# Optimization experiments

Measured on AMD Instinct MI355X. Metric: run time of the kernel, lower is better.

Reference implementation:

```python
import jax, jax.numpy as jnp
import numpy as np

D_IN = 128
HID = 129
D_H = HID - 1  # ttcn_dim = 128
N, L = 64, 128
NEG = -100000000.0


def setup_inputs() -> dict:
    key = jax.random.key(0)
    ks = jax.random.split(key, 10)
    x_int = jax.random.normal(ks[0], (N, L, D_IN), dtype=jnp.float32)
    mask_x = (jax.random.uniform(ks[1], (N, L, 1)) < 0.7).astype(jnp.float32)
    s1 = 1.0 / np.sqrt(D_IN)
    s2 = 1.0 / np.sqrt(D_H)
    W1 = jax.random.uniform(ks[2], (D_IN, D_H), minval=-s1, maxval=s1, dtype=jnp.float32)
    b1 = jax.random.uniform(ks[3], (D_H,), minval=-s1, maxval=s1, dtype=jnp.float32)
    W2 = jax.random.uniform(ks[4], (D_H, D_H), minval=-s2, maxval=s2, dtype=jnp.float32)
    b2 = jax.random.uniform(ks[5], (D_H,), minval=-s2, maxval=s2, dtype=jnp.float32)
    W3 = jax.random.uniform(ks[6], (D_H, D_IN * D_H), minval=-s2, maxval=s2, dtype=jnp.float32)
    b3 = jax.random.uniform(ks[7], (D_IN * D_H,), minval=-s2, maxval=s2, dtype=jnp.float32)
    t_bias = jax.random.normal(ks[8], (1, D_H), dtype=jnp.float32)
    return {"x_int": x_int, "mask_x": mask_x, "W1": W1, "b1": b1,
            "W2": W2, "b2": b2, "W3": W3, "b3": b3, "t_bias": t_bias}


def reference(x_int, mask_x, W1, b1, W2, b2, W3, b3, t_bias):
    n, lx, _ = x_int.shape
    # filter-generator MLP: (N, L, d_in) -> (N, L, d_in*d_h)
    h = jax.nn.relu(x_int @ W1 + b1)
    h = jax.nn.relu(h @ W2 + b2)
    filt = h @ W3 + b3
    # mask out unobserved timesteps, softmax over the time axis L
    filt = filt * mask_x + (1.0 - mask_x) * NEG
    p = jax.nn.softmax(filt, axis=-2)  # (N, L, d_in*d_h)
    p = p.reshape(n, lx, D_H, D_IN)    # (N, L, d_h, d_in)
    # broadcast-multiply-sum over L and d_in, fused as einsum
    out = jnp.einsum('nlf,nlhf->nh', x_int, p)
    return jax.nn.relu(out + t_bias)
```

## Files before the change

### kernel.cpp

```cpp
#include <hip/hip_runtime.h>

#define NH 16

using hfrag = __attribute__((ext_vector_type(8))) _Float16;
using f4v   = __attribute__((ext_vector_type(4))) float;

__global__ __launch_bounds__(256) void prep_kernel(
    const float* __restrict__ W3, _Float16* __restrict__ w3t,
    const float* __restrict__ x, float* __restrict__ xT,
    const float* __restrict__ maskx, float* __restrict__ xms,
    float* __restrict__ nmask) {
  __shared__ float t[32][33];
  __shared__ float sm2[2][128];
  const int bid = blockIdx.x;
  const int tx = threadIdx.x & 31, ty = threadIdx.x >> 5;
  if (bid < 2048) {
    const int f0 = (bid & 511) * 32;
    const int k0 = (bid >> 9) * 32;
#pragma unroll
    for (int i = 0; i < 4; ++i)
      t[ty + 8 * i][tx] = W3[(size_t)(k0 + ty + 8 * i) * 16384 + f0 + tx];
    __syncthreads();
#pragma unroll
    for (int i = 0; i < 4; ++i)
      w3t[(size_t)(f0 + ty + 8 * i) * 128 + k0 + tx] =
          (_Float16)(t[tx][ty + 8 * i] * 1.44269504f);
  } else if (bid < 3072) {
    const int b2 = bid - 2048;
    const int d0 = (b2 & 3) * 32, l0 = ((b2 >> 2) & 3) * 32, n = b2 >> 4;
    const size_t base = (size_t)n * 16384;
#pragma unroll
    for (int i = 0; i < 4; ++i)
      t[ty + 8 * i][tx] = x[base + (size_t)(l0 + ty + 8 * i) * 128 + d0 + tx];
    __syncthreads();
#pragma unroll
    for (int i = 0; i < 4; ++i)
      xT[base + (size_t)(d0 + ty + 8 * i) * 128 + l0 + tx] = t[tx][ty + 8 * i];
  } else {
    const int n = bid - 3072;
    const int d = threadIdx.x & 127, seg = threadIdx.x >> 7;
    const float* xn = x + (size_t)n * 16384;
    const float* mn = maskx + n * 128;
    float acc = 0.f;
#pragma unroll 8
    for (int l = seg * 64; l < seg * 64 + 64; ++l)
      acc += (mn[l] == 0.f) ? xn[l * 128 + d] : 0.f;
    sm2[seg][d] = acc;
    __syncthreads();
    if (threadIdx.x < 128) xms[n * 128 + d] = sm2[0][d] + sm2[1][d];
    if (threadIdx.x == 0) {
      float c = 0.f;
      for (int l = 0; l < 128; ++l) c += (mn[l] == 0.f) ? 1.f : 0.f;
      nmask[n] = c;
    }
  }
}

__global__ __launch_bounds__(256) void mlp2_kernel(
    const float* __restrict__ x, const float* __restrict__ W1,
    const float* __restrict__ b1, const float* __restrict__ W2,
    const float* __restrict__ b2, const float* __restrict__ maskx,
    _Float16* __restrict__ h2f) {
  __shared__ float wbuf[128 * 128];
  __shared__ float abuf[32 * 132];
  const int n = blockIdx.x, lq = blockIdx.y;
  const int tid = threadIdx.x;

  {
    const float4* wsrc = (const float4*)W1;
    float4* wdst = (float4*)wbuf;
#pragma unroll
    for (int i = 0; i < 16; ++i) wdst[tid + 256 * i] = wsrc[tid + 256 * i];
    const float4* xsrc = (const float4*)(x + (size_t)n * 16384 + lq * 32 * 128);
#pragma unroll
    for (int i = 0; i < 4; ++i) {
      int idx = tid + 256 * i;
      int row = idx >> 5, c4 = idx & 31;
      *(float4*)&abuf[row * 132 + c4 * 4] = xsrc[idx];
    }
  }
  __syncthreads();

  const int tl = tid >> 4, td = tid & 15;
  const int r0 = tl * 2, j0 = td * 8;
  const float m0 = maskx[n * 128 + lq * 32 + r0 + 0];
  const float m1 = maskx[n * 128 + lq * 32 + r0 + 1];
  float s[2][8];

#pragma unroll
  for (int i = 0; i < 2; ++i)
#pragma unroll
    for (int j = 0; j < 8; ++j) s[i][j] = 0.f;
#pragma unroll 4
  for (int k = 0; k < 128; ++k) {
    float a0 = abuf[(r0 + 0) * 132 + k];
    float a1 = abuf[(r0 + 1) * 132 + k];
    float4 bv0 = *(const float4*)&wbuf[k * 128 + j0];
    float4 bv1 = *(const float4*)&wbuf[k * 128 + j0 + 4];
    float b[8] = {bv0.x, bv0.y, bv0.z, bv0.w, bv1.x, bv1.y, bv1.z, bv1.w};
#pragma unroll
    for (int j = 0; j < 8; ++j) {
      s[0][j] += a0 * b[j];
      s[1][j] += a1 * b[j];
    }
  }
  __syncthreads();

#pragma unroll
  for (int i = 0; i < 2; ++i)
#pragma unroll
    for (int j = 0; j < 8; ++j)
      abuf[(r0 + i) * 132 + j0 + j] = fmaxf(s[i][j] + b1[j0 + j], 0.f);
  {
    const float4* wsrc = (const float4*)W2;
    float4* wdst = (float4*)wbuf;
#pragma unroll
    for (int i = 0; i < 16; ++i) wdst[tid + 256 * i] = wsrc[tid + 256 * i];
  }
  __syncthreads();

#pragma unroll
  for (int i = 0; i < 2; ++i)
#pragma unroll
    for (int j = 0; j < 8; ++j) s[i][j] = 0.f;
#pragma unroll 4
  for (int k = 0; k < 128; ++k) {
    float a0 = abuf[(r0 + 0) * 132 + k];
    float a1 = abuf[(r0 + 1) * 132 + k];
    float4 bv0 = *(const float4*)&wbuf[k * 128 + j0];
    float4 bv1 = *(const float4*)&wbuf[k * 128 + j0 + 4];
    float b[8] = {bv0.x, bv0.y, bv0.z, bv0.w, bv1.x, bv1.y, bv1.z, bv1.w};
#pragma unroll
    for (int j = 0; j < 8; ++j) {
      s[0][j] += a0 * b[j];
      s[1][j] += a1 * b[j];
    }
  }

  const float mm[2] = {m0, m1};
  const size_t obase = (size_t)n * 16384 + (size_t)(lq * 32) * 128;
#pragma unroll
  for (int i = 0; i < 2; ++i)
#pragma unroll
    for (int j = 0; j < 8; ++j)
      h2f[obase + (size_t)(r0 + i) * 128 + j0 + j] =
          (_Float16)(fmaxf(s[i][j] + b2[j0 + j], 0.f) * mm[i]);
}

__global__ __launch_bounds__(512, 2) void fused_mfma_kernel(
    const _Float16* __restrict__ h2f, const _Float16* __restrict__ w3t,
    const float* __restrict__ xT, const float* __restrict__ xms,
    const float* __restrict__ nmask, const float* __restrict__ tbias,
    float* __restrict__ out) {
  __shared__ _Float16 aLDS[128 * 128];
  __shared__ float wLDS[8][NH][16];
  const int n = blockIdx.x, hg = blockIdx.y;
  const int tid = threadIdx.x;
  const int wid = tid >> 6, lane = tid & 63;
  const int r = lane & 15, kg = lane >> 4;

  const _Float16* h2n = h2f + (size_t)n * 16384;
  {
    char* lb = (char*)aLDS;
#pragma unroll
    for (int i = 0; i < 4; ++i) {
      const int og = (tid + 512 * i) * 16;
      const int row = og >> 8;
      const int sl = (og >> 4) & 15;
      const float4 v = *(const float4*)((const char*)h2n + og);
      *(float4*)(lb + row * 256 + (sl ^ (row & 7)) * 16) = v;
    }
  }

  f4v xv[8];
  {
    const float* xc =
        xT + (size_t)n * 16384 + (size_t)(wid * 16 + r) * 128 + kg * 4;
#pragma unroll
    for (int rt = 0; rt < 8; ++rt) xv[rt] = *(const f4v*)(xc + rt * 16);
  }
  const float xm = xms[n * 128 + wid * 16 + r];
  const float nm = nmask[n];

  __syncthreads();

  hfrag af[4][8];
  {
    const char* lb = (const char*)aLDS;
#pragma unroll
    for (int ks = 0; ks < 4; ++ks) {
      const int dslByte = ((ks * 4 + kg) ^ (r & 7)) * 16;
#pragma unroll
      for (int rt = 0; rt < 8; ++rt)
        af[ks][rt] = *(const hfrag*)(lb + (rt * 16 + r) * 256 + dslByte);
    }
  }

  const _Float16* w3g =
      w3t + ((size_t)(hg * NH) * 128 + wid * 16 + r) * 128 + kg * 8;
  hfrag bcur[4];
#pragma unroll
  for (int ks = 0; ks < 4; ++ks) bcur[ks] = *(const hfrag*)(w3g + ks * 32);

#pragma unroll 2
  for (int h = 0; h < NH; ++h) {
    f4v acc[8];
#pragma unroll
    for (int rt = 0; rt < 8; ++rt) {
      f4v z = {0.f, 0.f, 0.f, 0.f};
      acc[rt] = __builtin_amdgcn_mfma_f32_16x16x32_f16(af[0][rt], bcur[0], z,
                                                       0, 0, 0);
    }
#pragma unroll
    for (int ks = 1; ks < 4; ++ks)
#pragma unroll
      for (int rt = 0; rt < 8; ++rt)
        acc[rt] = __builtin_amdgcn_mfma_f32_16x16x32_f16(af[ks][rt], bcur[ks],
                                                         acc[rt], 0, 0, 0);

    if (h + 1 < NH) {
      const _Float16* w3n = w3g + (size_t)(h + 1) * 16384;
#pragma unroll
      for (int ks = 0; ks < 4; ++ks) bcur[ks] = *(const hfrag*)(w3n + ks * 32);
    }

    float den0 = 0.f, den1 = 0.f, num0 = 0.f, num1 = 0.f;
#pragma unroll
    for (int rt = 0; rt < 8; rt += 2) {
#pragma unroll
      for (int j = 0; j < 4; ++j) {
        float e0 = __builtin_amdgcn_exp2f(acc[rt][j]);
        float e1 = __builtin_amdgcn_exp2f(acc[rt + 1][j]);
        den0 += e0;
        num0 += e0 * xv[rt][j];
        den1 += e1;
        num1 += e1 * xv[rt + 1][j];
      }
    }
    float den = den0 + den1, num = num0 + num1;
    den += __shfl_xor(den, 16);
    den += __shfl_xor(den, 32);
    num += __shfl_xor(num, 16);
    num += __shfl_xor(num, 32);
    den -= nm;
    num -= xm;
    if (kg == 0) wLDS[wid][h][r] = num * __builtin_amdgcn_rcpf(den);
  }

  __syncthreads();
  if (tid < 256) {
    const int rr = tid & 15, hh = tid >> 4;
    float s = 0.f;
#pragma unroll
    for (int w = 0; w < 8; ++w) s += wLDS[w][hh][rr];
    s += __shfl_xor(s, 1);
    s += __shfl_xor(s, 2);
    s += __shfl_xor(s, 4);
    s += __shfl_xor(s, 8);
    if (rr == 0) {
      const int h = hg * NH + hh;
      out[n * 128 + h] = fmaxf(s + tbias[h], 0.f);
    }
  }
}

extern "C" void kernel_launch(void* const* d_in, const int* in_sizes, int n_in,
                              void* d_out, int out_size, void* d_ws,
                              size_t ws_size, hipStream_t stream) {
  (void)in_sizes; (void)n_in; (void)out_size; (void)ws_size;
  const float* x     = (const float*)d_in[0];
  const float* maskx = (const float*)d_in[1];
  const float* W1    = (const float*)d_in[2];
  const float* b1    = (const float*)d_in[3];
  const float* W2    = (const float*)d_in[4];
  const float* b2    = (const float*)d_in[5];
  const float* W3    = (const float*)d_in[6];
  const float* tbias = (const float*)d_in[8];
  float* out = (float*)d_out;

  char* ws = (char*)d_ws;
  _Float16* w3t   = (_Float16*)ws;
  _Float16* h2f   = (_Float16*)(ws + (4u << 20));
  float*    xms   = (float*)(ws + (6u << 20));
  float*    nmask = (float*)(ws + (6u << 20) + (64u << 10));
  float*    xT    = (float*)(ws + (8u << 20));

  prep_kernel<<<3136, 256, 0, stream>>>(W3, w3t, x, xT, maskx, xms, nmask);
  mlp2_kernel<<<dim3(64, 4), 256, 0, stream>>>(x, W1, b1, W2, b2, maskx, h2f);
  fused_mfma_kernel<<<dim3(64, 8), 512, 0, stream>>>(h2f, w3t, xT, xms,
                                                     nmask, tbias, out);
}
```

Baseline: 74.75 us.

## Software-pipeline fused MFMA loop with dual accumulators and larger per-block head count

Doubles the number of output heads handled per block (NH 16→32) and halves the grid to match. The main loop becomes a two-stage software pipeline: two accumulator sets alternate so that one group's exp/softmax reduction overlaps the next group's MFMAs, with W3 fragments prefetched two steps ahead. To free registers for this, the A fragments are no longer held in registers; they are re-read from LDS for every MFMA. The aim is to hide softmax ALU and global-load latency behind matrix work, at the cost of much more LDS read traffic and fewer blocks to spread across CUs.

```diff
diff --git a/kernel.cpp b/kernel.cpp
--- a/kernel.cpp
+++ b/kernel.cpp
@@ -1,6 +1,6 @@
 #include <hip/hip_runtime.h>
 
-#define NH 16
+#define NH 32
 
 using hfrag = __attribute__((ext_vector_type(8))) _Float16;
 using f4v   = __attribute__((ext_vector_type(4))) float;
@@ -184,71 +184,87 @@
 
   __syncthreads();
 
-  hfrag af[4][8];
-  {
-    const char* lb = (const char*)aLDS;
-#pragma unroll
-    for (int ks = 0; ks < 4; ++ks) {
-      const int dslByte = ((ks * 4 + kg) ^ (r & 7)) * 16;
-#pragma unroll
-      for (int rt = 0; rt < 8; ++rt)
-        af[ks][rt] = *(const hfrag*)(lb + (rt * 16 + r) * 256 + dslByte);
-    }
-  }
+  const char* lb = (const char*)aLDS;
+  int dsl[4];
+#pragma unroll
+  for (int ks = 0; ks < 4; ++ks) dsl[ks] = ((ks * 4 + kg) ^ (r & 7)) * 16;
 
   const _Float16* w3g =
       w3t + ((size_t)(hg * NH) * 128 + wid * 16 + r) * 128 + kg * 8;
-  hfrag bcur[4];
-#pragma unroll
-  for (int ks = 0; ks < 4; ++ks) bcur[ks] = *(const hfrag*)(w3g + ks * 32);
-
-#pragma unroll 2
-  for (int h = 0; h < NH; ++h) {
-    f4v acc[8];
-#pragma unroll
-    for (int rt = 0; rt < 8; ++rt) {
-      f4v z = {0.f, 0.f, 0.f, 0.f};
-      acc[rt] = __builtin_amdgcn_mfma_f32_16x16x32_f16(af[0][rt], bcur[0], z,
-                                                       0, 0, 0);
-    }
-#pragma unroll
-    for (int ks = 1; ks < 4; ++ks)
-#pragma unroll
-      for (int rt = 0; rt < 8; ++rt)
-        acc[rt] = __builtin_amdgcn_mfma_f32_16x16x32_f16(af[ks][rt], bcur[ks],
-                                                         acc[rt], 0, 0, 0);
-
-    if (h + 1 < NH) {
-      const _Float16* w3n = w3g + (size_t)(h + 1) * 16384;
-#pragma unroll
-      for (int ks = 0; ks < 4; ++ks) bcur[ks] = *(const hfrag*)(w3n + ks * 32);
-    }
-
-    float den0 = 0.f, den1 = 0.f, num0 = 0.f, num1 = 0.f;
-#pragma unroll
-    for (int rt = 0; rt < 8; rt += 2) {
-#pragma unroll
-      for (int j = 0; j < 4; ++j) {
-        float e0 = __builtin_amdgcn_exp2f(acc[rt][j]);
-        float e1 = __builtin_amdgcn_exp2f(acc[rt + 1][j]);
-        den0 += e0;
-        num0 += e0 * xv[rt][j];
-        den1 += e1;
-        num1 += e1 * xv[rt + 1][j];
-      }
-    }
-    float den = den0 + den1, num = num0 + num1;
-    den += __shfl_xor(den, 16);
-    den += __shfl_xor(den, 32);
-    num += __shfl_xor(num, 16);
-    num += __shfl_xor(num, 32);
-    den -= nm;
-    num -= xm;
-    if (kg == 0) wLDS[wid][h][r] = num * __builtin_amdgcn_rcpf(den);
-  }
-
-  __syncthreads();
-  if (tid < 256) {
+
+#define AF(KS, RT) (*(const hfrag*)(lb + ((RT)*16 + r) * 256 + dsl[KS]))
+
+#define LOADB(B, H)                                                       \
+  do {                                                                    \
+    const _Float16* _p = w3g + (size_t)(H) * 16384;                       \
+    _Pragma("unroll") for (int ks = 0; ks < 4; ++ks) B[ks] =              \
+        *(const hfrag*)(_p + ks * 32);                                    \
+  } while (0)
+
+#define MFMA_GRP(ACC, B)                                                  \
+  do {                                                                    \
+    _Pragma("unroll") for (int rt = 0; rt < 8; ++rt) {                    \
+      f4v _z = {0.f, 0.f, 0.f, 0.f};                                      \
+      ACC[rt] = __builtin_amdgcn_mfma_f32_16x16x32_f16(AF(0, rt), B[0],   \
+                                                       _z, 0, 0, 0);      \
+    }                                                                     \
+    _Pragma("unroll") for (int ks = 1; ks < 4; ++ks)                      \
+        _Pragma("unroll") for (int rt = 0; rt < 8; ++rt) ACC[rt] =        \
+            __builtin_amdgcn_mfma_f32_16x16x32_f16(AF(ks, rt), B[ks],     \
+                                                   ACC[rt], 0, 0, 0);     \
+  } while (0)
+
+#define SMAX(ACC, H)                                                      \
+  do {                                                                    \
+    float den0 = 0.f, den1 = 0.f, num0 = 0.f, num1 = 0.f;                 \
+    _Pragma("unroll") for (int rt = 0; rt < 8; rt += 2) {                 \
+      _Pragma("unroll") for (int j = 0; j < 4; ++j) {                     \
+        float e0 = __builtin_amdgcn_exp2f(ACC[rt][j]);                    \
+        float e1 = __builtin_amdgcn_exp2f(ACC[rt + 1][j]);                 \
+        den0 += e0;                                                       \
+        num0 += e0 * xv[rt][j];                                           \
+        den1 += e1;                                                       \
+        num1 += e1 * xv[rt + 1][j];                                       \
+      }                                                                   \
+    }                                                                     \
+    float den = den0 + den1, num = num0 + num1;                           \
+    den += __shfl_xor(den, 16);                                           \
+    den += __shfl_xor(den, 32);                                           \
+    num += __shfl_xor(num, 16);                                           \
+    num += __shfl_xor(num, 32);                                           \
+    den -= nm;                                                            \
+    num -= xm;                                                            \
+    if (kg == 0) wLDS[wid][H][r] = num * __builtin_amdgcn_rcpf(den);      \
+  } while (0)
+
+  f4v accA[8], accB[8];
+  hfrag bA[4], bB[4];
+
+  LOADB(bA, 0);
+  LOADB(bB, 1);
+  MFMA_GRP(accA, bA);
+  LOADB(bA, 2);
+
+#pragma unroll 1
+  for (int h = 0; h < NH - 2; h += 2) {
+    MFMA_GRP(accB, bB);
+    LOADB(bB, h + 3);
+    SMAX(accA, h);
+    MFMA_GRP(accA, bA);
+    LOADB(bA, h + 4);
+    SMAX(accB, h + 1);
+  }
+  MFMA_GRP(accB, bB);
+  SMAX(accA, NH - 2);
+  SMAX(accB, NH - 1);
+
+#undef AF
+#undef LOADB
+#undef MFMA_GRP
+#undef SMAX
+
+  __syncthreads();
+  {
     const int rr = tid & 15, hh = tid >> 4;
     float s = 0.f;
 #pragma unroll
@@ -287,6 +303,6 @@
 
   prep_kernel<<<3136, 256, 0, stream>>>(W3, w3t, x, xT, maskx, xms, nmask);
   mlp2_kernel<<<dim3(64, 4), 256, 0, stream>>>(x, W1, b1, W2, b2, maskx, h2f);
-  fused_mfma_kernel<<<dim3(64, 8), 512, 0, stream>>>(h2f, w3t, xT, xms,
+  fused_mfma_kernel<<<dim3(64, 4), 512, 0, stream>>>(h2f, w3t, xT, xms,
                                                      nmask, tbias, out);
 }
```

Result: slower. 109.9 us (+47.0%).
